# Kernel optimization log

Measured on AMD Instinct MI355X. Metric: run time of the kernel, lower is better.

The kernel has to match this reference:

```python
import jax, jax.numpy as jnp
import numpy as np

# dims: B=1, T=2048 (prefill), dim=3072, Hq=32, Hkv=8, D=128, S=max_seq_len=4096

def _rotate_interleave(x):
    # (-x1, x0, -x3, x2, ...) pairwise rotation on last dim
    x = x.reshape(x.shape[:-1] + (-1, 2))
    x = jnp.stack((-x[..., 1], x[..., 0]), axis=-1)
    return x.reshape(x.shape[:-2] + (-1,))


def setup_inputs() -> dict:
    key = jax.random.key(0)
    ks = jax.random.split(key, 8)
    B, T, DIM, HQ, HKV, HD, S = 1, 2048, 3072, 32, 8, 128, 4096
    x = jax.random.normal(ks[0], (B, T, DIM), jnp.float32)
    wq = jax.random.normal(ks[1], (HQ * HD, DIM), jnp.float32) * 0.02
    wk = jax.random.normal(ks[2], (HKV * HD, DIM), jnp.float32) * 0.02
    wv = jax.random.normal(ks[3], (HKV * HD, DIM), jnp.float32) * 0.02
    wo = jax.random.normal(ks[4], (DIM, HQ * HD), jnp.float32) * 0.02
    freqs_cos = jax.random.uniform(ks[5], (T, HD), jnp.float32)
    freqs_sin = jax.random.uniform(ks[6], (T, HD), jnp.float32)
    input_pos = jnp.zeros((1,), jnp.int32)
    k_cache = jnp.zeros((1, S, HKV, HD), jnp.float32)
    v_cache = jnp.zeros((1, S, HKV, HD), jnp.float32)
    return {"x": x, "wq": wq, "wk": wk, "wv": wv, "wo": wo,
            "freqs_cos": freqs_cos, "freqs_sin": freqs_sin,
            "k_cache": k_cache, "v_cache": v_cache, "input_pos": input_pos}


def reference(x, wq, wk, wv, wo, freqs_cos, freqs_sin, k_cache, v_cache, input_pos):
    B, T, _ = x.shape
    HQ, HKV, HD = 32, 8, 128
    q = (x @ wq.T).reshape(B, T, HQ, HD)
    k = (x @ wk.T).reshape(B, T, HKV, HD)
    v = (x @ wv.T).reshape(B, T, HKV, HD)
    # interleaved RoPE (computed in fp32 as in apply_rotary_emb)
    fc = freqs_cos[None, :, None, :]
    fs = freqs_sin[None, :, None, :]
    q = q * fc + _rotate_interleave(q) * fs
    k = k * fc + _rotate_interleave(k) * fs
    # KV-cache update at start_pos (torch.ops.llama.update_cache)
    sp = input_pos[0]
    k_all = jax.lax.dynamic_update_slice(k_cache, k, (0, sp, 0, 0))  # [1,S,HKV,HD]
    v_all = jax.lax.dynamic_update_slice(v_cache, v, (0, sp, 0, 0))
    S = k_all.shape[1]
    # GQA: expand kv heads to match q heads (head h -> kv head h // rep)
    rep = HQ // HKV
    kr = jnp.repeat(k_all, rep, axis=2)  # [1,S,HQ,HD]
    vr = jnp.repeat(v_all, rep, axis=2)
    scale = 1.0 / np.sqrt(HD).astype(np.float32)
    scores = jnp.einsum('bthd,bshd->bhts', q, kr) * scale  # [B,HQ,T,S]
    # causal mask relative to start_pos (custom_sdpa is_causal=True path)
    qpos = sp + jnp.arange(T)
    kpos = jnp.arange(S)
    mask = kpos[None, :] <= qpos[:, None]                   # [T,S]
    scores = jnp.where(mask[None, None], scores, jnp.float32(-1e30))
    attn = jax.nn.softmax(scores, axis=-1)
    y = jnp.einsum('bhts,bshd->bthd', attn, vr).reshape(B, T, HQ * HD)
    return y @ wo.T
```

## Files before the change

### kernel.cpp

```cpp
#include <hip/hip_runtime.h>
#include <hip/hip_bf16.h>
#include <stdint.h>

typedef float f32x4 __attribute__((ext_vector_type(4)));
typedef short s16x8 __attribute__((ext_vector_type(8)));
typedef short s16x4 __attribute__((ext_vector_type(4)));
typedef unsigned short u16x2 __attribute__((ext_vector_type(2)));
typedef unsigned short u16x4 __attribute__((ext_vector_type(4)));

#define AS1 __attribute__((address_space(1)))
#define AS3 __attribute__((address_space(3)))

static constexpr int T_    = 2048;
static constexpr int DIM_  = 3072;
static constexpr int HQ_   = 32;
static constexpr int HKV_  = 8;
static constexpr int HD_   = 128;
static constexpr int S_    = 4096;
static constexpr int NQKV_ = HQ_ * HD_ + 2 * HKV_ * HD_;

__device__ __forceinline__ unsigned short f2b(float f) {
  return __builtin_bit_cast(unsigned short, __float2bfloat16(f));
}
__device__ __forceinline__ float b2f(unsigned short u) {
  return __bfloat162float(__builtin_bit_cast(__hip_bfloat16, u));
}
__device__ __forceinline__ float exp2a(float x) {
  float r; asm("v_exp_f32 %0, %1" : "=v"(r) : "v"(x)); return r;
}

__device__ __forceinline__ void gld_lds16(const void* g, void* l) {
  __builtin_amdgcn_global_load_lds((AS1 unsigned int*)(uintptr_t)g,
                                   (AS3 unsigned int*)l, 16, 0, 0);
}

#define FENCE() asm volatile("" ::: "memory")
#define BAR()   do { FENCE(); __builtin_amdgcn_s_barrier(); FENCE(); } while (0)
#define WAIT_VM(n)   asm volatile("s_waitcnt vmcnt(" #n ")" ::: "memory")
#define WAIT_LGKM(n) asm volatile("s_waitcnt lgkmcnt(" #n ")" ::: "memory")
#define SCHEDB()     __builtin_amdgcn_sched_barrier(0)

__global__ __launch_bounds__(256)
void k_cvt(const float* __restrict__ src, unsigned short* __restrict__ dst, int n4) {
  int i = blockIdx.x * 256 + threadIdx.x;
  if (i >= n4) return;
  float4 v = reinterpret_cast<const float4*>(src)[i];
  u16x4 o;
  o.x = f2b(v.x); o.y = f2b(v.y); o.z = f2b(v.z); o.w = f2b(v.w);
  reinterpret_cast<u16x4*>(dst)[i] = o;
}

__global__ __launch_bounds__(256)
void k_cvtW(const float* __restrict__ wq, const float* __restrict__ wk,
            const float* __restrict__ wv, unsigned short* __restrict__ dst) {
  int idx = blockIdx.x * 256 + threadIdx.x;
  if (idx >= 4718592) return;
  const float* src; int s;
  if (idx < 3145728)      { src = wq; s = idx; }
  else if (idx < 3932160) { src = wk; s = idx - 3145728; }
  else                    { src = wv; s = idx - 3932160; }
  float4 v = reinterpret_cast<const float4*>(src)[s];
  u16x4 o;
  o.x = f2b(v.x); o.y = f2b(v.y); o.z = f2b(v.z); o.w = f2b(v.w);
  reinterpret_cast<u16x4*>(dst)[idx] = o;
}

template<int BMT, bool OUT_BF16>
__global__ __launch_bounds__(512, 4)
void k_gemm192(const unsigned short* __restrict__ A,
               const unsigned short* __restrict__ B,
               void* __restrict__ Cout, int N, int K, int KT,
               int nbn, int xcdq) {
  constexpr int AROWS  = BMT / 64;
  constexpr int AFRAG  = BMT / 32;
  constexpr int LDSBUF = BMT * 128 + 24576;
  __shared__ char lds[2 * LDSBUF];
  const int bid = blockIdx.x;
  const int swz = (bid & 7) * xcdq + (bid >> 3);
  const int bm  = swz / nbn, bn = swz % nbn;
  const int tid = threadIdx.x, lane = tid & 63, wid = tid >> 6;
  const int wm  = wid >> 2, wn = wid & 3;
  const int r16 = lane & 15, q4 = lane >> 4;

  const unsigned short* Ag = A + (size_t)(bm * BMT) * K;
  const unsigned short* Bg = B + (size_t)(bn * 192) * K;

  const int srow = tid >> 3;
  const int scol = ((tid & 7) ^ (srow & 7)) * 8;

  f32x4 acc[AFRAG][3] = {};
  s16x8 af[AFRAG][2];

  auto stageA = [&](int c, int r, int t) {
    gld_lds16(Ag + (size_t)(r * 64 + srow) * K + t * 64 + scol,
              lds + c * LDSBUF + r * 8192 + tid * 16);
  };
  auto stageB = [&](int c, int r, int t) {
    gld_lds16(Bg + (size_t)(r * 64 + srow) * K + t * 64 + scol,
              lds + c * LDSBUF + BMT * 128 + r * 8192 + tid * 16);
  };
  auto readA = [&](int c) {
    #pragma unroll
    for (int i = 0; i < AFRAG; ++i) {
      const int arow = wm * (BMT / 2) + i * 16 + r16;
      #pragma unroll
      for (int kk = 0; kk < 2; ++kk)
        af[i][kk] = *(const s16x8*)(lds + c * LDSBUF + arow * 128 +
                                    (((kk * 4 + q4) ^ (arow & 7)) << 4));
    }
  };
  auto readB = [&](s16x8 (&dst)[2], int c, int j) {
    const int brow = wn * 48 + j * 16 + r16;
    #pragma unroll
    for (int kk = 0; kk < 2; ++kk)
      dst[kk] = *(const s16x8*)(lds + c * LDSBUF + BMT * 128 + brow * 128 +
                                (((kk * 4 + q4) ^ (brow & 7)) << 4));
  };

#define MFMA8(BF, J)                                                           \
  __builtin_amdgcn_s_setprio(1);                                               \
  _Pragma("unroll")                                                            \
  for (int i_ = 0; i_ < AFRAG; ++i_) {                                         \
    _Pragma("unroll")                                                          \
    for (int kk_ = 0; kk_ < 2; ++kk_)                                          \
      acc[i_][J] = __builtin_amdgcn_mfma_f32_16x16x32_bf16(                    \
          af[i_][kk_], BF[kk_], acc[i_][J], 0, 0, 0);                          \
  }                                                                            \
  __builtin_amdgcn_s_setprio(0);

  #pragma unroll
  for (int r = 0; r < AROWS; ++r) stageA(0, r, 0);
  stageB(0, 0, 0); stageB(0, 1, 0); stageB(0, 2, 0);
  WAIT_VM(0);
  BAR();

  for (int t = 0; t < KT; ++t) {
    const int c = t & 1;
    const bool hn = (t + 1 < KT);
    s16x8 bf0[2], bf1[2], bf2[2];
    readA(c);
    readB(bf0, c, 0);
    if (hn) {
      #pragma unroll
      for (int r = 0; r < AROWS; ++r) stageA(c ^ 1, r, t + 1);
      stageB(c ^ 1, 0, t + 1); stageB(c ^ 1, 1, t + 1); stageB(c ^ 1, 2, t + 1);
    }
    readB(bf1, c, 1);
    WAIT_LGKM(2); SCHEDB();
    MFMA8(bf0, 0);
    readB(bf2, c, 2);
    WAIT_LGKM(2); SCHEDB();
    MFMA8(bf1, 1);
    WAIT_LGKM(0); SCHEDB();
    MFMA8(bf2, 2);
    if (hn) WAIT_VM(0);
    BAR();
  }
#undef MFMA8

  #pragma unroll
  for (int i = 0; i < AFRAG; ++i) {
    const int row = bm * BMT + wm * (BMT / 2) + i * 16 + q4 * 4;
    #pragma unroll
    for (int j = 0; j < 3; ++j) {
      const int col = bn * 192 + wn * 48 + j * 16 + r16;
      if constexpr (OUT_BF16) {
        unsigned short* C = (unsigned short*)Cout;
        #pragma unroll
        for (int rr = 0; rr < 4; ++rr)
          C[(size_t)(row + rr) * N + col] = f2b(acc[i][j][rr]);
      } else {
        float* C = (float*)Cout;
        #pragma unroll
        for (int rr = 0; rr < 4; ++rr)
          C[(size_t)(row + rr) * N + col] = acc[i][j][rr];
      }
    }
  }
}

__global__ __launch_bounds__(256)
void k_prep(const unsigned short* __restrict__ qkv,
            const float* __restrict__ fc, const float* __restrict__ fs,
            const float* __restrict__ kc, const float* __restrict__ vc,
            unsigned short* __restrict__ Qr, unsigned short* __restrict__ Kall,
            unsigned short* __restrict__ VT, const int* __restrict__ ipos) {
  __shared__ unsigned short lds[64][136];
  const int b = blockIdx.x, tid = threadIdx.x;

  if (b < 4096) {
    int idx = b * 256 + tid;
    int t   = idx >> 9;
    int rem = idx & 511;
    int h   = rem >> 4;
    int c8  = (rem & 15) << 3;
    s16x8 xv = *(const s16x8*)(qkv + (size_t)t * NQKV_ + h * HD_ + c8);
    float4 ca = *(const float4*)(fc + t * HD_ + c8);
    float4 cb = *(const float4*)(fc + t * HD_ + c8 + 4);
    float4 sa = *(const float4*)(fs + t * HD_ + c8);
    float4 sb = *(const float4*)(fs + t * HD_ + c8 + 4);
    float cc[8] = {ca.x, ca.y, ca.z, ca.w, cb.x, cb.y, cb.z, cb.w};
    float ss[8] = {sa.x, sa.y, sa.z, sa.w, sb.x, sb.y, sb.z, sb.w};
    s16x8 o;
    #pragma unroll
    for (int i = 0; i < 4; ++i) {
      float x0 = b2f((unsigned short)xv[2 * i]);
      float x1 = b2f((unsigned short)xv[2 * i + 1]);
      o[2 * i]     = (short)f2b(x0 * cc[2 * i]     - x1 * ss[2 * i]);
      o[2 * i + 1] = (short)f2b(x1 * cc[2 * i + 1] + x0 * ss[2 * i + 1]);
    }
    *(s16x8*)(Qr + ((size_t)h * T_ + t) * HD_ + c8) = o;

  } else if (b < 5120) {
    int idx = (b - 4096) * 256 + tid;
    int t   = idx >> 7;
    int rem = idx & 127;
    int hk  = rem >> 4;
    int c8  = (rem & 15) << 3;
    int sp  = ipos[0];
    s16x8 xv = *(const s16x8*)(qkv + (size_t)t * NQKV_ + HQ_ * HD_ + hk * HD_ + c8);
    float4 ca = *(const float4*)(fc + t * HD_ + c8);
    float4 cb = *(const float4*)(fc + t * HD_ + c8 + 4);
    float4 sa = *(const float4*)(fs + t * HD_ + c8);
    float4 sb = *(const float4*)(fs + t * HD_ + c8 + 4);
    float cc[8] = {ca.x, ca.y, ca.z, ca.w, cb.x, cb.y, cb.z, cb.w};
    float ss[8] = {sa.x, sa.y, sa.z, sa.w, sb.x, sb.y, sb.z, sb.w};
    s16x8 o;
    #pragma unroll
    for (int i = 0; i < 4; ++i) {
      float x0 = b2f((unsigned short)xv[2 * i]);
      float x1 = b2f((unsigned short)xv[2 * i + 1]);
      o[2 * i]     = (short)f2b(x0 * cc[2 * i]     - x1 * ss[2 * i]);
      o[2 * i + 1] = (short)f2b(x1 * cc[2 * i + 1] + x0 * ss[2 * i + 1]);
    }
    *(s16x8*)(Kall + ((size_t)hk * S_ + sp + t) * HD_ + c8) = o;

  } else if (b < 5376) {
    int bb = b - 5120;
    int hk = bb >> 5;
    int tt = bb & 31;
    int sp = ipos[0];
    #pragma unroll
    for (int p = 0; p < 4; ++p) {
      int e   = p * 256 + tid;
      int tr  = e >> 4;
      int col = (e & 15) << 3;
      *reinterpret_cast<s16x8*>(&lds[tr][col]) =
          *reinterpret_cast<const s16x8*>(&qkv[(size_t)(tt * 64 + tr) * NQKV_ +
                                               (HQ_ + HKV_) * HD_ + hk * HD_ + col]);
    }
    __syncthreads();
    #pragma unroll
    for (int p = 0; p < 32; ++p) {
      int e = p * 256 + tid;
      int d = e >> 6;
      int t = e & 63;
      VT[((size_t)hk * HD_ + d) * S_ + sp + tt * 64 + t] = lds[t][d];
    }

  } else {
    int sp = ipos[0];
    int total = sp * HKV_ * HD_;
    for (int idx = (b - 5376) * 256 + tid; idx < total; idx += 256 * 256) {
      int s   = idx >> 10;
      int rem = idx & 1023;
      int hk  = rem >> 7;
      int d   = rem & 127;
      Kall[((size_t)hk * S_ + s) * HD_ + d] = f2b(kc[((size_t)s * HKV_ + hk) * HD_ + d]);
      VT[((size_t)hk * HD_ + d) * S_ + s]   = f2b(vc[((size_t)s * HKV_ + hk) * HD_ + d]);
    }
  }
}

__global__ __launch_bounds__(256, 2)
void k_attn(const unsigned short* __restrict__ Qr,
            const unsigned short* __restrict__ Kall,
            const unsigned short* __restrict__ VT,
            unsigned short* __restrict__ Y,
            const int* __restrict__ ipos) {
  constexpr int QB = 64, KB = 64;
  __shared__ char lds[65536];
  const int bid  = blockIdx.x;
  const int hk   = bid & 7;
  const int u    = bid >> 3;
  const int pr   = u & 1;
  const int qt   = 31 - (u >> 1);
  const int h0   = hk * 4 + pr * 2;
  const int tid  = threadIdx.x, lane = tid & 63, wave = tid >> 6;
  const int r16  = lane & 15, q4 = lane >> 4;
  const int vx   = r16 & 7;
  const float NEG_INF = -__builtin_inff();
  const float MINIT   = -1.0e30f;

  const int sp = ipos[0];
  const int qbase = qt * QB + wave * 16;
  const unsigned short* Kbase = Kall + (size_t)hk * S_ * HD_;
  const unsigned short* Vbase = VT + (size_t)hk * HD_ * S_;

  s16x8 qf0[4], qf1[4];
  {
    const unsigned short* qp0 = Qr + ((size_t)h0 * T_ + qbase + r16) * HD_;
    const unsigned short* qp1 = qp0 + (size_t)T_ * HD_;
    #pragma unroll
    for (int ki = 0; ki < 4; ++ki) {
      qf0[ki] = *reinterpret_cast<const s16x8*>(qp0 + ki * 32 + q4 * 8);
      qf1[ki] = *reinterpret_cast<const s16x8*>(qp1 + ki * 32 + q4 * 8);
    }
  }
  SCHEDB(); WAIT_VM(0); SCHEDB();

  auto stage = [&](int c, int jt) {
    #pragma unroll
    for (int p = 0; p < 4; ++p) {
      int e  = p * 256 + tid;
      int kr = e >> 4;
      int ks = (e & 15) ^ (kr & 7);
      gld_lds16(Kbase + (size_t)(jt * KB + kr) * HD_ + ks * 8,
                lds + c * 16384 + e * 16);
    }
    #pragma unroll
    for (int p = 0; p < 4; ++p) {
      int e  = p * 256 + tid;
      int vd = e >> 3;
      int vs = (e & 7) ^ (vd & 7);
      gld_lds16(Vbase + (size_t)vd * S_ + jt * KB + vs * 8,
                lds + 32768 + c * 16384 + e * 16);
    }
  };

  f32x4 o0[8] = {}, o1[8] = {};
  float m0 = MINIT, l0 = 0.f, m1 = MINIT, l1 = 0.f;
  const int qpos = sp + qbase + r16;
  const int qpos_wave_max = sp + qbase + 15;
  int jmax = (sp + qt * QB + QB - 1) >> 6;
  if (jmax > S_ / KB - 1) jmax = S_ / KB - 1;
  const float scale2 = 0.12751744416312068f;

  stage(0, 0);

  for (int j = 0; j <= jmax; ++j) {
    const int c = j & 1;
    if (j < jmax) { stage(c ^ 1, j + 1); WAIT_VM(8); }
    else         { WAIT_VM(0); }
    BAR();

    const bool active = (j * KB <= qpos_wave_max);
    if (active) {
      const char* kb = lds + c * 16384;
      const char* vb = lds + 32768 + c * 16384;
      const bool needMask = (j * KB + KB - 1) > (sp + qbase);

      auto headPass = [&](const s16x8 (&qf)[4], f32x4 (&o)[8],
                          float& m, float& l) {
        f32x4 sfr[4];
        __builtin_amdgcn_s_setprio(1);
        #pragma unroll
        for (int fn = 0; fn < 4; ++fn) {
          sfr[fn] = f32x4{0.f, 0.f, 0.f, 0.f};
          #pragma unroll
          for (int ki = 0; ki < 4; ++ki) {
            s16x8 kf = *(const s16x8*)(kb + (fn * 16 + r16) * 256 +
                                       (((ki * 4 + q4) ^ vx) << 4));
            sfr[fn] = __builtin_amdgcn_mfma_f32_16x16x32_bf16(kf, qf[ki], sfr[fn], 0, 0, 0);
          }
        }
        __builtin_amdgcn_s_setprio(0);
        float p[16];
        if (needMask) {
          const int kbp = j * KB + q4 * 4;
          #pragma unroll
          for (int fn = 0; fn < 4; ++fn)
            #pragma unroll
            for (int r = 0; r < 4; ++r)
              p[fn * 4 + r] = (kbp + fn * 16 + r <= qpos) ? sfr[fn][r] * scale2 : NEG_INF;
        } else {
          #pragma unroll
          for (int fn = 0; fn < 4; ++fn)
            #pragma unroll
            for (int r = 0; r < 4; ++r)
              p[fn * 4 + r] = sfr[fn][r] * scale2;
        }
        float t0 = fmaxf(p[0], p[1]),  t1 = fmaxf(p[2], p[3]);
        float t2 = fmaxf(p[4], p[5]),  t3 = fmaxf(p[6], p[7]);
        float t4 = fmaxf(p[8], p[9]),  t5 = fmaxf(p[10], p[11]);
        float t6 = fmaxf(p[12], p[13]), t7 = fmaxf(p[14], p[15]);
        float pmax = fmaxf(fmaxf(fmaxf(t0, t1), fmaxf(t2, t3)),
                           fmaxf(fmaxf(t4, t5), fmaxf(t6, t7)));
        pmax = fmaxf(pmax, __shfl_xor(pmax, 16));
        pmax = fmaxf(pmax, __shfl_xor(pmax, 32));
        if (!__all(pmax <= m + 8.0f)) {
          float mn = fmaxf(m, pmax);
          float alpha = exp2a(m - mn);
          m = mn; l *= alpha;
          #pragma unroll
          for (int r = 0; r < 4; ++r) {
            float aq = __shfl(alpha, q4 * 4 + r);
            #pragma unroll
            for (int db = 0; db < 8; ++db) o[db][r] *= aq;
          }
        }
        float rs = 0.f;
        #pragma unroll
        for (int i = 0; i < 16; ++i) { p[i] = exp2a(p[i] - m); rs += p[i]; }
        rs += __shfl_xor(rs, 16); rs += __shfl_xor(rs, 32);
        l += rs;
        s16x8 pf[2];
        #pragma unroll
        for (int w = 0; w < 2; ++w)
          #pragma unroll
          for (int i = 0; i < 8; ++i)
            pf[w][i] = (short)f2b(p[w * 8 + i]);
        const int voff = (q4 & 1) * 8;
        const int sbase = q4 >> 1;
        __builtin_amdgcn_s_setprio(1);
        #pragma unroll
        for (int w = 0; w < 2; ++w) {
          #pragma unroll
          for (int db = 0; db < 8; ++db) {
            const char* vr = vb + (db * 16 + r16) * 128 + voff;
            s16x4 va  = *(const s16x4*)(vr + (((w * 4 + sbase) ^ vx) << 4));
            s16x4 vb2 = *(const s16x4*)(vr + (((w * 4 + 2 + sbase) ^ vx) << 4));
            s16x8 vf = __builtin_shufflevector(va, vb2, 0, 1, 2, 3, 4, 5, 6, 7);
            o[db] = __builtin_amdgcn_mfma_f32_16x16x32_bf16(pf[w], vf, o[db], 0, 0, 0);
          }
        }
        __builtin_amdgcn_s_setprio(0);
      };

      headPass(qf0, o0, m0, l0);
      headPass(qf1, o1, m1, l1);
    }
    BAR();
  }

  {
    float rcpl0 = 1.0f / l0, rcpl1 = 1.0f / l1;
    float rl0[4], rl1[4];
    #pragma unroll
    for (int r = 0; r < 4; ++r) {
      rl0[r] = __shfl(rcpl0, q4 * 4 + r);
      rl1[r] = __shfl(rcpl1, q4 * 4 + r);
    }
    #pragma unroll
    for (int db = 0; db < 8; ++db)
      #pragma unroll
      for (int r = 0; r < 4; ++r) {
        int t = qt * QB + wave * 16 + q4 * 4 + r;
        int d = db * 16 + r16;
        Y[(size_t)t * (HQ_ * HD_) + h0 * HD_ + d]       = f2b(o0[db][r] * rl0[r]);
        Y[(size_t)t * (HQ_ * HD_) + (h0 + 1) * HD_ + d] = f2b(o1[db][r] * rl1[r]);
      }
  }
}

extern "C" void kernel_launch(void* const* d_in, const int* in_sizes, int n_in,
                              void* d_out, int out_size, void* d_ws, size_t ws_size,
                              hipStream_t stream) {
  const float* x  = (const float*)d_in[0];
  const float* wq = (const float*)d_in[1];
  const float* wk = (const float*)d_in[2];
  const float* wv = (const float*)d_in[3];
  const float* wo = (const float*)d_in[4];
  const float* fc = (const float*)d_in[5];
  const float* fs = (const float*)d_in[6];
  const float* kc = (const float*)d_in[7];
  const float* vc = (const float*)d_in[8];
  const int* ipos = (const int*)d_in[9];

  char* ws = (char*)d_ws;
  unsigned short* xb   = (unsigned short*)(ws);
  unsigned short* wqkv = (unsigned short*)(ws + 12582912);
  unsigned short* qkv  = (unsigned short*)(ws + 50331648);
  unsigned short* Qr   = (unsigned short*)(ws + 75497472);
  unsigned short* Kall = (unsigned short*)(ws + 92274688);
  unsigned short* VT   = (unsigned short*)(ws + 100663296);
  unsigned short* wo_b = (unsigned short*)(ws);
  unsigned short* y    = qkv;

  k_cvt<<<6144, 256, 0, stream>>>(x, xb, 6291456 / 4);
  k_cvtW<<<18432, 256, 0, stream>>>(wq, wk, wv, wqkv);

  k_gemm192<128, true><<<512, 512, 0, stream>>>(xb, wqkv, qkv, NQKV_, DIM_, 48, 32, 64);

  k_cvt<<<12288, 256, 0, stream>>>(wo, wo_b, 12582912 / 4);

  k_prep<<<5632, 256, 0, stream>>>(qkv, fc, fs, kc, vc, Qr, Kall, VT, ipos);

  k_attn<<<512, 256, 0, stream>>>(Qr, Kall, VT, y, ipos);

  k_gemm192<64, false><<<512, 512, 0, stream>>>(y, wo_b, d_out, DIM_, HQ_ * HD_, 64, 16, 64);
}
```

Before: 280.9 us.

## Tile attention as one head over 128 queries instead of two heads

```diff
diff --git a/kernel.cpp b/kernel.cpp
--- a/kernel.cpp
+++ b/kernel.cpp
@@ -278,14 +278,13 @@
             const unsigned short* __restrict__ VT,
             unsigned short* __restrict__ Y,
             const int* __restrict__ ipos) {
-  constexpr int QB = 64, KB = 64;
+  constexpr int QB = 128, KB = 64;
   __shared__ char lds[65536];
   const int bid  = blockIdx.x;
   const int hk   = bid & 7;
   const int u    = bid >> 3;
-  const int pr   = u & 1;
-  const int qt   = 31 - (u >> 1);
-  const int h0   = hk * 4 + pr * 2;
+  const int h    = hk * 4 + (u & 3);
+  const int qt   = 15 - (u >> 2);
   const int tid  = threadIdx.x, lane = tid & 63, wave = tid >> 6;
   const int r16  = lane & 15, q4 = lane >> 4;
   const int vx   = r16 & 7;
@@ -293,18 +292,18 @@
   const float MINIT   = -1.0e30f;
 
   const int sp = ipos[0];
-  const int qbase = qt * QB + wave * 16;
+  const int qbase = qt * QB + wave * 32;
   const unsigned short* Kbase = Kall + (size_t)hk * S_ * HD_;
   const unsigned short* Vbase = VT + (size_t)hk * HD_ * S_;
 
-  s16x8 qf0[4], qf1[4];
+  s16x8 qfA[4], qfB[4];
   {
-    const unsigned short* qp0 = Qr + ((size_t)h0 * T_ + qbase + r16) * HD_;
-    const unsigned short* qp1 = qp0 + (size_t)T_ * HD_;
+    const unsigned short* qpA = Qr + ((size_t)h * T_ + qbase + r16) * HD_;
+    const unsigned short* qpB = qpA + 16 * HD_;
     #pragma unroll
     for (int ki = 0; ki < 4; ++ki) {
-      qf0[ki] = *reinterpret_cast<const s16x8*>(qp0 + ki * 32 + q4 * 8);
-      qf1[ki] = *reinterpret_cast<const s16x8*>(qp1 + ki * 32 + q4 * 8);
+      qfA[ki] = *reinterpret_cast<const s16x8*>(qpA + ki * 32 + q4 * 8);
+      qfB[ki] = *reinterpret_cast<const s16x8*>(qpB + ki * 32 + q4 * 8);
     }
   }
   SCHEDB(); WAIT_VM(0); SCHEDB();
@@ -328,10 +327,12 @@
     }
   };
 
-  f32x4 o0[8] = {}, o1[8] = {};
-  float m0 = MINIT, l0 = 0.f, m1 = MINIT, l1 = 0.f;
-  const int qpos = sp + qbase + r16;
-  const int qpos_wave_max = sp + qbase + 15;
+  f32x4 oA[8] = {}, oB[8] = {};
+  float mA = MINIT, lA = 0.f, mB = MINIT, lB = 0.f;
+  const int qposA = sp + qbase + r16;
+  const int qposB = qposA + 16;
+  const int maxA  = sp + qbase + 15;
+  const int maxB  = maxA + 16;
   int jmax = (sp + qt * QB + QB - 1) >> 6;
   if (jmax > S_ / KB - 1) jmax = S_ / KB - 1;
   const float scale2 = 0.12751744416312068f;
@@ -344,28 +345,39 @@
     else         { WAIT_VM(0); }
     BAR();
 
-    const bool active = (j * KB <= qpos_wave_max);
-    if (active) {
+    const bool actA = (j * KB <= maxA);
+    const bool actB = (j * KB <= maxB);
+    if (actB) {
       const char* kb = lds + c * 16384;
       const char* vb = lds + 32768 + c * 16384;
-      const bool needMask = (j * KB + KB - 1) > (sp + qbase);
-
-      auto headPass = [&](const s16x8 (&qf)[4], f32x4 (&o)[8],
-                          float& m, float& l) {
-        f32x4 sfr[4];
-        __builtin_amdgcn_s_setprio(1);
+      f32x4 sfrA[4], sfrB[4];
+      __builtin_amdgcn_s_setprio(1);
+      #pragma unroll
+      for (int fn = 0; fn < 4; ++fn) {
+        sfrA[fn] = f32x4{0.f, 0.f, 0.f, 0.f};
+        sfrB[fn] = f32x4{0.f, 0.f, 0.f, 0.f};
         #pragma unroll
-        for (int fn = 0; fn < 4; ++fn) {
-          sfr[fn] = f32x4{0.f, 0.f, 0.f, 0.f};
+        for (int ki = 0; ki < 4; ++ki) {
+          s16x8 kf = *(const s16x8*)(kb + (fn * 16 + r16) * 256 +
+                                     (((ki * 4 + q4) ^ vx) << 4));
+          sfrA[fn] = __builtin_amdgcn_mfma_f32_16x16x32_bf16(kf, qfA[ki], sfrA[fn], 0, 0, 0);
+          sfrB[fn] = __builtin_amdgcn_mfma_f32_16x16x32_bf16(kf, qfB[ki], sfrB[fn], 0, 0, 0);
+        }
+      }
+      __builtin_amdgcn_s_setprio(0);
+
+      s16x8 pfA[2], pfB[2];
+      auto softmax = [&](const f32x4 (&sfr)[4], int qpos, float& m, float& l,
+                         f32x4 (&o)[8], s16x8 (&pf)[2], bool act) {
+        float p[16];
+        if (!act) {
           #pragma unroll
-          for (int ki = 0; ki < 4; ++ki) {
-            s16x8 kf = *(const s16x8*)(kb + (fn * 16 + r16) * 256 +
-                                       (((ki * 4 + q4) ^ vx) << 4));
-            sfr[fn] = __builtin_amdgcn_mfma_f32_16x16x32_bf16(kf, qf[ki], sfr[fn], 0, 0, 0);
-          }
+          for (int w = 0; w < 2; ++w)
+            #pragma unroll
+            for (int i = 0; i < 8; ++i) pf[w][i] = 0;
+          return;
         }
-        __builtin_amdgcn_s_setprio(0);
-        float p[16];
+        const bool needMask = (j * KB + KB - 1) > (qpos - r16);
         if (needMask) {
           const int kbp = j * KB + q4 * 4;
           #pragma unroll
@@ -404,51 +416,51 @@
         for (int i = 0; i < 16; ++i) { p[i] = exp2a(p[i] - m); rs += p[i]; }
         rs += __shfl_xor(rs, 16); rs += __shfl_xor(rs, 32);
         l += rs;
-        s16x8 pf[2];
         #pragma unroll
         for (int w = 0; w < 2; ++w)
           #pragma unroll
           for (int i = 0; i < 8; ++i)
             pf[w][i] = (short)f2b(p[w * 8 + i]);
-        const int voff = (q4 & 1) * 8;
-        const int sbase = q4 >> 1;
-        __builtin_amdgcn_s_setprio(1);
+      };
+      softmax(sfrA, qposA, mA, lA, oA, pfA, actA);
+      softmax(sfrB, qposB, mB, lB, oB, pfB, true);
+
+      const int voff = (q4 & 1) * 8;
+      const int sbase = q4 >> 1;
+      __builtin_amdgcn_s_setprio(1);
+      #pragma unroll
+      for (int w = 0; w < 2; ++w) {
         #pragma unroll
-        for (int w = 0; w < 2; ++w) {
-          #pragma unroll
-          for (int db = 0; db < 8; ++db) {
-            const char* vr = vb + (db * 16 + r16) * 128 + voff;
-            s16x4 va  = *(const s16x4*)(vr + (((w * 4 + sbase) ^ vx) << 4));
-            s16x4 vb2 = *(const s16x4*)(vr + (((w * 4 + 2 + sbase) ^ vx) << 4));
-            s16x8 vf = __builtin_shufflevector(va, vb2, 0, 1, 2, 3, 4, 5, 6, 7);
-            o[db] = __builtin_amdgcn_mfma_f32_16x16x32_bf16(pf[w], vf, o[db], 0, 0, 0);
-          }
+        for (int db = 0; db < 8; ++db) {
+          const char* vr = vb + (db * 16 + r16) * 128 + voff;
+          s16x4 va  = *(const s16x4*)(vr + (((w * 4 + sbase) ^ vx) << 4));
+          s16x4 vb2 = *(const s16x4*)(vr + (((w * 4 + 2 + sbase) ^ vx) << 4));
+          s16x8 vf = __builtin_shufflevector(va, vb2, 0, 1, 2, 3, 4, 5, 6, 7);
+          oA[db] = __builtin_amdgcn_mfma_f32_16x16x32_bf16(pfA[w], vf, oA[db], 0, 0, 0);
+          oB[db] = __builtin_amdgcn_mfma_f32_16x16x32_bf16(pfB[w], vf, oB[db], 0, 0, 0);
         }
-        __builtin_amdgcn_s_setprio(0);
-      };
-
-      headPass(qf0, o0, m0, l0);
-      headPass(qf1, o1, m1, l1);
+      }
+      __builtin_amdgcn_s_setprio(0);
     }
     BAR();
   }
 
   {
-    float rcpl0 = 1.0f / l0, rcpl1 = 1.0f / l1;
-    float rl0[4], rl1[4];
+    float rcA = 1.0f / lA, rcB = 1.0f / lB;
+    float rlA[4], rlB[4];
     #pragma unroll
     for (int r = 0; r < 4; ++r) {
-      rl0[r] = __shfl(rcpl0, q4 * 4 + r);
-      rl1[r] = __shfl(rcpl1, q4 * 4 + r);
+      rlA[r] = __shfl(rcA, q4 * 4 + r);
+      rlB[r] = __shfl(rcB, q4 * 4 + r);
     }
     #pragma unroll
     for (int db = 0; db < 8; ++db)
       #pragma unroll
       for (int r = 0; r < 4; ++r) {
-        int t = qt * QB + wave * 16 + q4 * 4 + r;
-        int d = db * 16 + r16;
-        Y[(size_t)t * (HQ_ * HD_) + h0 * HD_ + d]       = f2b(o0[db][r] * rl0[r]);
-        Y[(size_t)t * (HQ_ * HD_) + (h0 + 1) * HD_ + d] = f2b(o1[db][r] * rl1[r]);
+        int tA = qt * QB + wave * 32 + q4 * 4 + r;
+        int d  = db * 16 + r16;
+        Y[(size_t)tA * (HQ_ * HD_) + h * HD_ + d]        = f2b(oA[db][r] * rlA[r]);
+        Y[(size_t)(tA + 16) * (HQ_ * HD_) + h * HD_ + d] = f2b(oB[db][r] * rlB[r]);
       }
   }
 }
```

Result: faster. 258.3 us (-8.1%).
